# Kernel tuning notes

Measured on AMD Instinct MI355X. Metric: run time of the kernel, lower is better.

Reference implementation:

```python
import jax, jax.numpy as jnp
from jax import lax
import numpy as np


def _conv(x, w, stride):
    # x: [B,C,D,H,W], w: [3,3,3,Cin,Cout]; kernel 3, pad 1 (matches SubMConv3d / SparseConv3d(3, s, padding=1))
    return lax.conv_general_dilated(x, w, (stride, stride, stride), [(1, 1)] * 3,
                                    dimension_numbers=('NCDHW', 'DHWIO', 'NCDHW'))


def _bn_relu(y, scale, shift, mask):
    # eval-mode BatchNorm folded to scale/shift, ReLU, then restrict to active sites
    return jnp.maximum(y * scale[None, :, None, None, None] + shift[None, :, None, None, None], 0.0) * mask


def _downsample_mask(m):
    # SparseConv3d(k=3, s=2, p=1): output site active iff any input in its 3x3x3 window is active
    return lax.reduce_window(m, -jnp.inf, lax.max, (1, 1, 3, 3, 3), (1, 1, 2, 2, 2),
                             [(0, 0), (0, 0), (1, 1), (1, 1), (1, 1)])


def setup_inputs() -> dict:
    key = jax.random.key(0)
    ks = jax.random.split(key, 40)
    B, D = 1, 128
    occ = jax.random.uniform(ks[0], (B, 1, D, D, D)) < 0.05
    x = jax.random.normal(ks[1], (B, 16, D, D, D), jnp.float32) * occ

    def w(k, ci, co):
        return jax.random.normal(k, (3, 3, 3, ci, co), jnp.float32) * (1.0 / np.sqrt(27.0 * ci))

    def sc(k, c):
        return jax.random.uniform(k, (c,), jnp.float32, 0.5, 1.5)

    def sh(k, c):
        return jax.random.normal(k, (c,), jnp.float32) * 0.1

    chans = [(16, 16), (16, 16), (16, 32), (32, 32), (32, 32), (32, 64), (64, 64), (64, 64), (64, 64)]
    names = ['w0a', 'w0b', 'wd0', 'w1a', 'w1b', 'wd1', 'w2a', 'w2b', 'w2c']
    d = {'x': x, 'mask': occ}
    i = 2
    for n, (ci, co) in zip(names, chans):
        d[n] = w(ks[i], ci, co)
        d['s' + n[1:]] = sc(ks[i + 1], co)
        d['b' + n[1:]] = sh(ks[i + 2], co)
        i += 3
    return d


def reference(x, mask, w0a, s0a, b0a, w0b, s0b, b0b, wd0, sd0, bd0,
              w1a, s1a, b1a, w1b, s1b, b1b, wd1, sd1, bd1,
              w2a, s2a, b2a, w2b, s2b, b2b, w2c, s2c, b2c):
    m0 = mask.astype(x.dtype)                       # active sites at full res [B,1,128,128,128]
    h = _bn_relu(_conv(x, w0a, 1), s0a, b0a, m0)    # conv0 (subm0)
    h = _bn_relu(_conv(h, w0b, 1), s0b, b0b, m0)
    m1 = _downsample_mask(m0)                       # down0 activity [B,1,64,64,64]
    h = _bn_relu(_conv(h, wd0, 2), sd0, bd0, m1)
    h = _bn_relu(_conv(h, w1a, 1), s1a, b1a, m1)    # conv1 (subm1)
    h = _bn_relu(_conv(h, w1b, 1), s1b, b1b, m1)
    m2 = _downsample_mask(m1)                       # down1 activity [B,1,32,32,32]
    h = _bn_relu(_conv(h, wd1, 2), sd1, bd1, m2)
    h = _bn_relu(_conv(h, w2a, 1), s2a, b2a, m2)    # conv2 (subm2)
    h = _bn_relu(_conv(h, w2b, 1), s2b, b2b, m2)
    h = _bn_relu(_conv(h, w2c, 1), s2c, b2c, m2)
    return h                                        # .dense() -> [B,64,32,32,32]
```

## Files before the change

### kernel.cpp

```cpp
#include <hip/hip_runtime.h>
#include <cstdint>

typedef unsigned short u16;
typedef unsigned int u32;
typedef unsigned char u8;
typedef unsigned long long u64;
typedef __attribute__((ext_vector_type(8))) short short8;
typedef __attribute__((ext_vector_type(4))) float f32x4;

#define CAP 131072

__device__ __forceinline__ float bf1(u16 v){ union{u32 i; float f;} c; c.i = ((u32)v) << 16; return c.f; }
__device__ __forceinline__ u16 f2bf(float f){
    union{float f; u32 i;} c; c.f = f; u32 i = c.i;
    return (u16)((i + 0x7FFFu + ((i >> 16) & 1u)) >> 16);
}
__device__ __forceinline__ u16 bits2bf(u32 b){ union{u32 i; float f;} c; c.i = b; return f2bf(c.f); }

constexpr int ilog2c(int n){ return n <= 1 ? 0 : 1 + ilog2c(n / 2); }

struct PAll {
    const void* w[9];
    u32 wstart[10];
    int cin[9], cout[9], mode[9];
    const void* s[18];
};

__global__ __launch_bounds__(256)
void prepact_k(PAll J, u16* __restrict__ FR, float* __restrict__ S,
               const u16* __restrict__ s0a_probe, u32* __restrict__ flag,
               const void* __restrict__ xv, u64* __restrict__ bmask,
               u32* __restrict__ bcnt, u16* __restrict__ Xp){
    int ok = 1;
    #pragma unroll
    for (int i = 0; i < 8; i += 2){
        u16 vv = s0a_probe[i];
        if (vv < 0x3F00u || vv > 0x3FC0u) ok = 0;
    }
    const u32 isbf = ok ? 1u : 0u;

    if (blockIdx.x < 8192){
        const int v = blockIdx.x * 256 + threadIdx.x;
        const size_t N = 2097152;
        u16 vals[16];
        u32 a = 0;
        if (isbf) {
            const u16* x = (const u16*)xv;
            #pragma unroll
            for (int c = 0; c < 16; ++c){
                const u16 b = x[(size_t)c * N + v];
                vals[c] = b;
                a |= (u32)b & 0x7FFFu;
            }
        } else {
            const u32* x = (const u32*)xv;
            #pragma unroll
            for (int c = 0; c < 16; ++c){
                const u32 b = x[(size_t)c * N + v];
                vals[c] = bits2bf(b);
                a |= b & 0x7FFFFFFFu;
            }
        }
        const bool act = (a != 0);
        const u64 m = __ballot(act);
        __shared__ u32 wc[4];
        const int lane = threadIdx.x & 63, wv = threadIdx.x >> 6;
        if (lane == 0) { bmask[v >> 6] = m; wc[wv] = (u32)__popcll(m); }
        __syncthreads();
        if (threadIdx.x == 0) bcnt[blockIdx.x] = wc[0] + wc[1] + wc[2] + wc[3];
        if (act){
            u32 wbase = 0;
            for (int i = 0; i < wv; ++i) wbase += wc[i];
            const u32 local = wbase + (u32)__popcll(m & ((1ull << lane) - 1ull));
            u16* dst = Xp + ((size_t)blockIdx.x * 256 + local) * 16;
            *(short8*)(dst)     = *(const short8*)(vals);
            *(short8*)(dst + 8) = *(const short8*)(vals + 8);
        }
        return;
    }

    const int gi = (int)(blockIdx.x - 8192) * 256 + threadIdx.x;
    if (gi == 0) flag[0] = isbf;

    const int wtot = (int)J.wstart[9];
    if (gi < wtot){
        int j = 0;
        while (gi >= (int)J.wstart[j + 1]) ++j;
        const int i = gi - (int)J.wstart[j];
        const void* w = J.w[j];
        const int CIN = J.cin[j], COUT = J.cout[j];
        const int jj = i & 7;
        const int lane = (i >> 3) & 63;
        int rest = i >> 9;
        int src = -1;
        if (J.mode[j] == 0){
            const int KC = CIN >> 5, NT = COUT >> 4;
            const int nt = rest % NT; rest /= NT;
            const int kc = rest % KC; const int tap = rest / KC;
            const int k = kc * 32 + (lane >> 4) * 8 + jj;
            const int co = nt * 16 + (lane & 15);
            src = (tap * CIN + k) * COUT + co;
        } else if (J.mode[j] == 1){
            const int nt = rest & 1; const int pair = rest >> 1;
            const int kg = (lane >> 4) * 8 + jj;
            const int tap = pair * 2 + (kg >> 4);
            const int ci = kg & 15;
            const int co = nt * 16 + (lane & 15);
            if (tap < 27) src = (tap * 16 + ci) * 32 + co;
        } else {
            const int pair = rest;
            const int kg = (lane >> 4) * 8 + jj;
            const int tap = pair * 2 + (kg >> 4);
            const int ci = kg & 15;
            const int co = lane & 15;
            if (tap < 27) src = (tap * 16 + ci) * 16 + co;
        }
        float v = 0.f;
        if (src >= 0) v = isbf ? bf1(((const u16*)w)[src]) : ((const float*)w)[src];
        FR[gi] = f2bf(v);
    } else {
        const int i2 = gi - wtot;
        const int len[18] = {16,16,16,16,32,32,32,32,32,32,64,64,64,64,64,64,64,64};
        const int off[18] = {0,16,32,48,64,96,128,160,192,224,256,320,384,448,512,576,640,704};
        if (i2 < 768){
            int b = 0, base = 0;
            while (i2 >= base + len[b]) { base += len[b]; ++b; }
            const int t = i2 - base;
            const float v = isbf ? bf1(((const u16*)J.s[b])[t]) : ((const float*)J.s[b])[t];
            S[off[b] + t] = v;
        }
    }
}

__global__ __launch_bounds__(1024)
void aux_k(const u32* __restrict__ bcnt, u32* __restrict__ boff, u32* __restrict__ cnt,
           const u64* __restrict__ bmask, u8* __restrict__ m1){
    if (blockIdx.x == 0){
        __shared__ u32 lds[1024];
        const int t = threadIdx.x;
        u32 loc[8]; u32 s = 0;
        #pragma unroll
        for (int i = 0; i < 8; ++i){ loc[i] = s; s += bcnt[t * 8 + i]; }
        lds[t] = s;
        __syncthreads();
        u32 v = s;
        for (int d = 1; d < 1024; d <<= 1){
            u32 o = (t >= d) ? lds[t - d] : 0;
            __syncthreads();
            v += o; lds[t] = v;
            __syncthreads();
        }
        const u32 base = v - s;
        #pragma unroll
        for (int i = 0; i < 8; ++i) boff[t * 8 + i] = base + loc[i];
        if (t == 1023) cnt[0] = v;
    } else {
        const int v = (blockIdx.x - 1) * 1024 + threadIdx.x;
        const int xo = v & 63, yo = (v >> 6) & 63, zo = v >> 12;
        u32 a = 0;
        #pragma unroll
        for (int kz = 0; kz < 3; ++kz){ const int iz = 2*zo + kz - 1; if ((unsigned)iz >= 128u) continue;
          #pragma unroll
          for (int ky = 0; ky < 3; ++ky){ const int iy = 2*yo + ky - 1; if ((unsigned)iy >= 128u) continue;
            #pragma unroll
            for (int kx = 0; kx < 3; ++kx){ const int ix = 2*xo + kx - 1; if ((unsigned)ix >= 128u) continue;
              const int vv = (iz * 128 + iy) * 128 + ix;
              a |= (u32)((bmask[vv >> 6] >> (vv & 63)) & 1ull);
        }}}
        m1[v] = (u8)a;
    }
}

__global__ __launch_bounds__(256)
void scatter2m_k(const u16* __restrict__ Xp, const u64* __restrict__ bmask,
                 const u32* __restrict__ boff, int* __restrict__ idxmap,
                 int* __restrict__ alist, u16* __restrict__ f,
                 const u8* __restrict__ m1, u8* __restrict__ m2){
    if (blockIdx.x < 8192){
        const int v = blockIdx.x * 256 + threadIdx.x;
        const int lane = threadIdx.x & 63, wv = threadIdx.x >> 6;
        const u64 m = bmask[v >> 6];
        __shared__ u32 wc[4];
        if (lane == 0) wc[wv] = (u32)__popcll(m);
        __syncthreads();
        u32 wbase = 0;
        for (int i = 0; i < wv; ++i) wbase += wc[i];
        const bool act = (m >> lane) & 1ull;
        const u32 rank = (u32)__popcll(m & ((1ull << lane) - 1ull));
        int slot = -1;
        if (act){
            const u32 sl = boff[blockIdx.x] + wbase + rank;
            if (sl < CAP){
                slot = (int)sl;
                alist[slot] = v;
                const u16* src = Xp + ((size_t)blockIdx.x * 256 + wbase + rank) * 16;
                u16* dst = f + (size_t)slot * 16;
                *(short8*)(dst)     = *(const short8*)(src);
                *(short8*)(dst + 8) = *(const short8*)(src + 8);
            }
        }
        idxmap[v] = slot;
    } else {
        const int v = (int)(blockIdx.x - 8192) * 256 + threadIdx.x;
        const int xo = v & 31, yo = (v >> 5) & 31, zo = v >> 10;
        u8 a = 0;
        #pragma unroll
        for (int kz = 0; kz < 3; ++kz){ const int iz = 2*zo + kz - 1; if ((unsigned)iz >= 64u) continue;
          #pragma unroll
          for (int ky = 0; ky < 3; ++ky){ const int iy = 2*yo + ky - 1; if ((unsigned)iy >= 64u) continue;
            #pragma unroll
            for (int kx = 0; kx < 3; ++kx){ const int ix = 2*xo + kx - 1; if ((unsigned)ix >= 64u) continue;
              a |= m1[((size_t)iz * 64 + iy) * 64 + ix];
        }}}
        m2[v] = a;
    }
}

__global__ __launch_bounds__(256)
void sconvm_k(const u16* __restrict__ fin, const int* __restrict__ idxmap,
              const int* __restrict__ alist, const u32* __restrict__ cnt,
              const u16* __restrict__ wf, const float* __restrict__ sc,
              const float* __restrict__ sh, u16* __restrict__ fout){
    const int n = min((int)cnt[0], CAP);
    const int j = blockIdx.x * 4 + (threadIdx.x >> 6);
    const int sbase = j * 16;
    if (sbase >= n) return;
    const int lane = threadIdx.x & 63;
    const int m = lane & 15, quad = lane >> 4;

    const int s = sbase + m;
    const int v = (s < n) ? alist[s] : -1;
    int xo = 0, yo = 0, zo = 0;
    if (v >= 0){ xo = v & 127; yo = (v >> 7) & 127; zo = v >> 14; }

    f32x4 acc = {0.f,0.f,0.f,0.f};
    #pragma unroll
    for (int p = 0; p < 14; ++p){
        const int tp = p * 2 + (quad >> 1);
        short8 a = {0,0,0,0,0,0,0,0};
        if (v >= 0 && tp < 27){
            const int kz = tp / 9, ky = (tp / 3) % 3, kx = tp % 3;
            const int iz = zo + kz - 1, iy = yo + ky - 1, ix = xo + kx - 1;
            if ((unsigned)iz < 128u && (unsigned)iy < 128u && (unsigned)ix < 128u){
                const int sn = idxmap[((size_t)iz * 128 + iy) * 128 + ix];
                if (sn >= 0) a = *(const short8*)(fin + (size_t)sn * 16 + (quad & 1) * 8);
            }
        }
        short8 b = *(const short8*)(wf + ((size_t)p * 64 + lane) * 8);
        acc = __builtin_amdgcn_mfma_f32_16x16x32_bf16(a, b, acc, 0, 0, 0);
    }

    const int co = lane & 15;
    const float scl = sc[co], shf = sh[co];
    #pragma unroll
    for (int r = 0; r < 4; ++r){
        const int srow = sbase + quad * 4 + r;
        if (srow < n){
            fout[(size_t)srow * 16 + co] = f2bf(fmaxf(acc[r] * scl + shf, 0.f));
        }
    }
}

__global__ __launch_bounds__(256)
void convd0m_k(const u16* __restrict__ fbuf, const int* __restrict__ idxmap,
               const u16* __restrict__ wf, const float* __restrict__ sc,
               const float* __restrict__ sh, const u8* __restrict__ mk,
               u16* __restrict__ out)
{
    const int wj = blockIdx.x * 4 + (threadIdx.x >> 6);
    const int lane = threadIdx.x & 63;
    const int m = lane & 15, quad = lane >> 4;
    const int xo_b = (wj & 3) * 16;
    const int yo = (wj >> 2) & 63;
    const int zo = wj >> 8;

    f32x4 acc0 = {0.f,0.f,0.f,0.f}, acc1 = {0.f,0.f,0.f,0.f};
    const int ix_m = (xo_b + m) * 2 - 1;

    #pragma unroll
    for (int p = 0; p < 14; ++p){
        const int tp = p * 2 + (quad >> 1);
        short8 a = {0,0,0,0,0,0,0,0};
        if (tp < 27){
            const int kz = tp / 9, ky = (tp / 3) % 3, kx = tp % 3;
            const int iz = 2*zo + kz - 1, iy = 2*yo + ky - 1, ix = ix_m + kx;
            if ((unsigned)iz < 128u && (unsigned)iy < 128u && (unsigned)ix < 128u){
                const int sn = idxmap[((size_t)iz * 128 + iy) * 128 + ix];
                if (sn >= 0) a = *(const short8*)(fbuf + (size_t)sn * 16 + (quad & 1) * 8);
            }
        }
        short8 b0 = *(const short8*)(wf + ((size_t)(p*2+0) * 64 + lane) * 8);
        short8 b1 = *(const short8*)(wf + ((size_t)(p*2+1) * 64 + lane) * 8);
        acc0 = __builtin_amdgcn_mfma_f32_16x16x32_bf16(a, b0, acc0, 0, 0, 0);
        acc1 = __builtin_amdgcn_mfma_f32_16x16x32_bf16(a, b1, acc1, 0, 0, 0);
    }

    const int vb = wj * 16 + quad * 4;
    const u32 m4 = *(const u32*)(mk + vb);
    const int n = lane & 15;
    #pragma unroll
    for (int nt = 0; nt < 2; ++nt){
        const int co = nt * 16 + n;
        const float s = sc[co], h = sh[co];
        const f32x4 acc = nt ? acc1 : acc0;
        #pragma unroll
        for (int r = 0; r < 4; ++r){
            float val = fmaxf(acc[r] * s + h, 0.f);
            val = ((m4 >> (8*r)) & 0xFFu) ? val : 0.f;
            out[(size_t)(vb + r) * 32 + co] = f2bf(val);
        }
    }
}

template<int DIN, int DOUT, int CIN, int COUT, int STRIDE, bool FINAL>
__global__ __launch_bounds__(256)
void mconv_k(const u16* __restrict__ in, const u16* __restrict__ wf,
             const float* __restrict__ sc, const float* __restrict__ sh,
             const u8* __restrict__ mk, void* __restrict__ out,
             const u32* __restrict__ flag)
{
    constexpr int KC = CIN / 32;
    constexpr int NT = COUT / 16;
    constexpr int XT = DOUT / 16;
    const int wj = blockIdx.x * 4 + (threadIdx.x >> 6);
    const int lane = threadIdx.x & 63;
    const int m = lane & 15, quad = lane >> 4;

    const int xo_b = (wj % XT) * 16;
    const int yo = (wj / XT) % DOUT;
    const int zo = wj / (XT * DOUT);

    f32x4 acc[NT];
    #pragma unroll
    for (int i = 0; i < NT; ++i) acc[i] = (f32x4){0.f,0.f,0.f,0.f};

    const int ix0 = (xo_b + m) * STRIDE - 1;
    for (int kz = 0; kz < 3; ++kz){
      const int iz = zo * STRIDE + kz - 1;
      if ((unsigned)iz >= (unsigned)DIN) continue;
      for (int ky = 0; ky < 3; ++ky){
        const int iy = yo * STRIDE + ky - 1;
        if ((unsigned)iy >= (unsigned)DIN) continue;
        const size_t rowb = ((size_t)iz * DIN + iy) * DIN;
        #pragma unroll
        for (int kx = 0; kx < 3; ++kx){
          const int ix = ix0 + kx;
          const bool v = (unsigned)ix < (unsigned)DIN;
          const int tap = (kz*3 + ky)*3 + kx;
          const u16* ap = in + (rowb + ix) * CIN + quad * 8;
          const u16* bp = wf + (size_t)tap * KC * NT * 512 + lane * 8;
          #pragma unroll
          for (int kc = 0; kc < KC; ++kc){
            short8 a = {0,0,0,0,0,0,0,0};
            if (v) a = *(const short8*)(ap + kc * 32);
            #pragma unroll
            for (int nt = 0; nt < NT; ++nt){
              short8 b = *(const short8*)(bp + (kc * NT + nt) * 512);
              acc[nt] = __builtin_amdgcn_mfma_f32_16x16x32_bf16(a, b, acc[nt], 0, 0, 0);
            }
          }
    }}}

    const int vb = wj * 16 + quad * 4;
    const u32 m4 = *(const u32*)(mk + vb);
    const int n = lane & 15;
    #pragma unroll
    for (int nt = 0; nt < NT; ++nt){
        const int co = nt * 16 + n;
        const float s = sc[co], h = sh[co];
        #pragma unroll
        for (int r = 0; r < 4; ++r){
            float val = fmaxf(acc[nt][r] * s + h, 0.f);
            val = ((m4 >> (8*r)) & 0xFFu) ? val : 0.f;
            ((u16*)out)[(size_t)(vb + r) * COUT + co] = f2bf(val);
        }
    }
    (void)flag;
}

template<int D, int CIN, int COUT, bool FINAL>
__global__ __launch_bounds__((D/32)*4*64)
void mconvw_k(const u16* __restrict__ in, const u16* __restrict__ wf,
              const float* __restrict__ sc, const float* __restrict__ sh,
              const u8* __restrict__ mk, void* __restrict__ out,
              const u32* __restrict__ flag)
{
    constexpr int KC = CIN / 32;
    constexpr int NT = COUT / 16;
    constexpr int CH8 = CIN / 8;
    constexpr int WPR = D / 32;
    constexpr int BT = WPR * 4 * 64;
    __shared__ u16 tile[16 * 2048];

    const int t = threadIdx.x;
    const int yp = blockIdx.x % (D / 2);
    const int zp = blockIdx.x / (D / 2);

    #pragma unroll
    for (int ri = 0; ri < 16; ++ri){
        const int dz = ri >> 2, jy = ri & 3;
        const int iz = 2*zp + dz - 1, iy = 2*yp + jy - 1;
        if ((unsigned)iz < (unsigned)D && (unsigned)iy < (unsigned)D){
            const u16* src = in + ((size_t)(iz * D + iy) * D) * CIN;
            u16* dst = &tile[ri * 2048];
            for (int c = t; c < D * CH8; c += BT){
                const int x = c / CH8, c8 = c % CH8;
                *(short8*)(dst + (c8 * D + x) * 8) = *(const short8*)(src + c * 8);
            }
        }
    }
    __syncthreads();

    const int lane = t & 63, w = t >> 6;
    const int r = w / WPR;
    const int r2z = r >> 1, r2y = r & 1;
    const int xo_b = (w % WPR) * 32;
    const int zo = 2*zp + r2z, yo = 2*yp + r2y;
    const int m = lane & 15, quad = lane >> 4;

    f32x4 acc0[NT], acc1[NT];
    #pragma unroll
    for (int i = 0; i < NT; ++i){ acc0[i] = (f32x4){0.f,0.f,0.f,0.f}; acc1[i] = (f32x4){0.f,0.f,0.f,0.f}; }

    #pragma unroll
    for (int kz = 0; kz < 3; ++kz){
      const int iz = zo + kz - 1;
      if ((unsigned)iz >= (unsigned)D) continue;
      #pragma unroll
      for (int ky = 0; ky < 3; ++ky){
        const int iy = yo + ky - 1;
        if ((unsigned)iy >= (unsigned)D) continue;
        const u16* row = &tile[((r2z + kz) * 4 + (r2y + ky)) * 2048];
        #pragma unroll
        for (int kx = 0; kx < 3; ++kx){
          const int ix0 = xo_b + m + kx - 1;
          const int ix1 = ix0 + 16;
          const bool aok0 = (unsigned)ix0 < (unsigned)D;
          const bool aok1 = (unsigned)ix1 < (unsigned)D;
          const int tap = (kz * 3 + ky) * 3 + kx;
          const u16* bp = wf + (size_t)tap * KC * NT * 512 + lane * 8;
          #pragma unroll
          for (int kc = 0; kc < KC; ++kc){
            short8 a0 = {0,0,0,0,0,0,0,0};
            short8 a1 = {0,0,0,0,0,0,0,0};
            if (aok0) a0 = *(const short8*)(row + ((kc * 4 + quad) * D + ix0) * 8);
            if (aok1) a1 = *(const short8*)(row + ((kc * 4 + quad) * D + ix1) * 8);
            #pragma unroll
            for (int nt = 0; nt < NT; ++nt){
              short8 b = *(const short8*)(bp + (kc * NT + nt) * 512);
              acc0[nt] = __builtin_amdgcn_mfma_f32_16x16x32_bf16(a0, b, acc0[nt], 0, 0, 0);
              acc1[nt] = __builtin_amdgcn_mfma_f32_16x16x32_bf16(a1, b, acc1[nt], 0, 0, 0);
            }
          }
        }
      }
    }

    const int base = (zo * D + yo) * D;
    const int vb0 = base + xo_b + quad * 4;
    const int vb1 = vb0 + 16;
    const u32 m4_0 = *(const u32*)(mk + vb0);
    const u32 m4_1 = *(const u32*)(mk + vb1);
    const int n = lane & 15;
    if (FINAL) {
        const bool bfout = flag[0] != 0;
        #pragma unroll
        for (int nt = 0; nt < NT; ++nt){
            const int co = nt * 16 + n;
            const float s = sc[co], h = sh[co];
            float4 o0, o1;
            float* p0 = &o0.x; float* p1 = &o1.x;
            #pragma unroll
            for (int r4 = 0; r4 < 4; ++r4){
                float v0 = fmaxf(acc0[nt][r4] * s + h, 0.f);
                float v1 = fmaxf(acc1[nt][r4] * s + h, 0.f);
                p0[r4] = ((m4_0 >> (8*r4)) & 0xFFu) ? v0 : 0.f;
                p1[r4] = ((m4_1 >> (8*r4)) & 0xFFu) ? v1 : 0.f;
            }
            if (!bfout) {
                *(float4*)((float*)out + (size_t)co * (D*D*D) + vb0) = o0;
                *(float4*)((float*)out + (size_t)co * (D*D*D) + vb1) = o1;
            } else {
                u16* ob0 = (u16*)out + (size_t)co * (D*D*D) + vb0;
                u16* ob1 = (u16*)out + (size_t)co * (D*D*D) + vb1;
                #pragma unroll
                for (int r4 = 0; r4 < 4; ++r4){ ob0[r4] = f2bf(p0[r4]); ob1[r4] = f2bf(p1[r4]); }
            }
        }
    } else {
        #pragma unroll
        for (int nt = 0; nt < NT; ++nt){
            const int co = nt * 16 + n;
            const float s = sc[co], h = sh[co];
            #pragma unroll
            for (int r4 = 0; r4 < 4; ++r4){
                float v0 = fmaxf(acc0[nt][r4] * s + h, 0.f);
                float v1 = fmaxf(acc1[nt][r4] * s + h, 0.f);
                v0 = ((m4_0 >> (8*r4)) & 0xFFu) ? v0 : 0.f;
                v1 = ((m4_1 >> (8*r4)) & 0xFFu) ? v1 : 0.f;
                ((u16*)out)[(size_t)(vb0 + r4) * COUT + co] = f2bf(v0);
                ((u16*)out)[(size_t)(vb1 + r4) * COUT + co] = f2bf(v1);
            }
        }
    }
}

extern "C" void kernel_launch(void* const* d_in, const int* in_sizes, int n_in,
                              void* d_out, int out_size, void* d_ws, size_t ws_size,
                              hipStream_t stream)
{
    (void)out_size; (void)ws_size;

    int wb = 2;
    for (int i = 1; i < n_in; ++i) { if (in_sizes[i] == 6912) { wb = i; break; } }

    const void* x = d_in[0];
    const void *w0a=d_in[wb+0],  *s0a=d_in[wb+1],  *b0a=d_in[wb+2];
    const void *w0b=d_in[wb+3],  *s0b=d_in[wb+4],  *b0b=d_in[wb+5];
    const void *wd0=d_in[wb+6],  *sd0=d_in[wb+7],  *bd0=d_in[wb+8];
    const void *w1a=d_in[wb+9],  *s1a=d_in[wb+10], *b1a=d_in[wb+11];
    const void *w1b=d_in[wb+12], *s1b=d_in[wb+13], *b1b=d_in[wb+14];
    const void *wd1=d_in[wb+15], *sd1=d_in[wb+16], *bd1=d_in[wb+17];
    const void *w2a=d_in[wb+18], *s2a=d_in[wb+19], *b2a=d_in[wb+20];
    const void *w2b=d_in[wb+21], *s2b=d_in[wb+22], *b2b=d_in[wb+23];
    const void *w2c=d_in[wb+24], *s2c=d_in[wb+25], *b2c=d_in[wb+26];

    char* ws = (char*)d_ws;
    int*   idxmap = (int*)(ws);
    u16*   Fb0    = (u16*)(ws + 8388608);
    u16*   Fb1    = (u16*)(ws + 12582912);
    u16*   Fb2    = (u16*)(ws + 16777216);
    u16*   Rb1    = (u16*)(ws + 25165824);
    u16*   Rb2    = (u16*)(ws + 41943040);
    u8*    m1     = (u8*)(ws + 58720256);
    u8*    m2     = (u8*)(ws + 58982400);
    u32*   cnt    = (u32*)(ws + 59015168);
    int*   alist  = (int*)(ws + 59015424);
    u16*   FR     = (u16*)(ws + 59539712);
    float* S      = (float*)(ws + 60483328);
    u32*   flag   = (u32*)(ws + 60486400);
    u64*   bmask  = (u64*)(ws + 60486656);
    u32*   bcnt   = (u32*)(ws + 60748800);
    u32*   boff   = (u32*)(ws + 60781568);
    u16*   Xp     = (u16*)(ws + 67108864);

    u16* wfs0a = FR + 0;
    u16* wfs0b = FR + 7168;
    u16* fd0   = FR + 14336;
    u16* f1a   = FR + 28672;
    u16* f1b   = FR + 56320;
    u16* fd1   = FR + 83968;
    u16* f2a   = FR + 139264;
    u16* f2b   = FR + 249856;
    u16* f2c   = FR + 360448;

    PAll J;
    const void* jsrc[9] = {w0a, w0b, wd0, w1a, w1b, wd1, w2a, w2b, w2c};
    const u32 jlen[9]   = {7168,7168,14336,27648,27648,55296,110592,110592,110592};
    const int jcin[9]   = {16,16,16,32,32,32,64,64,64};
    const int jcout[9]  = {16,16,32,32,32,64,64,64,64};
    const int jmode[9]  = {2,2,1,0,0,0,0,0,0};
    u32 acc = 0;
    for (int i = 0; i < 9; ++i){
        J.w[i] = jsrc[i]; J.wstart[i] = acc; acc += jlen[i];
        J.cin[i] = jcin[i]; J.cout[i] = jcout[i]; J.mode[i] = jmode[i];
    }
    J.wstart[9] = acc;
    const void* sv[18] = {s0a,b0a,s0b,b0b,sd0,bd0,s1a,b1a,s1b,b1b,sd1,bd1,s2a,b2a,s2b,b2b,s2c,b2c};
    for (int i = 0; i < 18; ++i) J.s[i] = sv[i];
    const u32 ptot = acc + 768;
    const int prep_blocks = (int)((ptot + 255) / 256);

    float *cs0a=S+0,  *cb0a=S+16,  *cs0b=S+32,  *cb0b=S+48;
    float *csd0=S+64, *cbd0=S+96,  *cs1a=S+128, *cb1a=S+160, *cs1b=S+192, *cb1b=S+224;
    float *csd1=S+256,*cbd1=S+320, *cs2a=S+384, *cb2a=S+448, *cs2b=S+512, *cb2b=S+576, *cs2c=S+640, *cb2c=S+704;

    prepact_k<<<8192 + prep_blocks, 256, 0, stream>>>(J, FR, S, (const u16*)s0a, flag,
                                                      x, bmask, bcnt, Xp);
    aux_k<<<257, 1024, 0, stream>>>(bcnt, boff, cnt, bmask, m1);
    scatter2m_k<<<8320, 256, 0, stream>>>(Xp, bmask, boff, idxmap, alist, Fb0, m1, m2);

    sconvm_k<<<2048, 256, 0, stream>>>(Fb0, idxmap, alist, cnt, wfs0a, cs0a, cb0a, Fb1);
    sconvm_k<<<2048, 256, 0, stream>>>(Fb1, idxmap, alist, cnt, wfs0b, cs0b, cb0b, Fb2);
    convd0m_k<<<4096, 256, 0, stream>>>(Fb2, idxmap, fd0, csd0, cbd0, m1, Rb1);
    mconvw_k<64,32,32,false><<<1024, 512, 0, stream>>>(Rb1, f1a, cs1a, cb1a, m1, Rb2, flag);
    mconvw_k<64,32,32,false><<<1024, 512, 0, stream>>>(Rb2, f1b, cs1b, cb1b, m1, Rb1, flag);
    mconv_k<64,32,32,64,2,false><<<512, 256, 0, stream>>>(Rb1, fd1, csd1, cbd1, m2, Rb2, flag);
    mconvw_k<32,64,64,false><<<256, 256, 0, stream>>>(Rb2, f2a, cs2a, cb2a, m2, Rb1, flag);
    mconvw_k<32,64,64,false><<<256, 256, 0, stream>>>(Rb1, f2b, cs2b, cb2b, m2, Rb2, flag);
    mconvw_k<32,64,64,true ><<<256, 256, 0, stream>>>(Rb2, f2c, cs2c, cb2c, m2, d_out, flag);
}
```

Measured before the change: 485.2 us.

## Replace block scan with atomic offsets and fuse tail convs into cooperative kernel

Removes the separate aux kernel's block-count prefix scan by having each block reserve its compaction slots with an atomicAdd on a global counter. Computes m2 directly from the full-resolution bitmask instead of from m1, so m1 and m2 are built in the same scatter kernel. Fuses the last four dense 32^3 convolutions into one cooperative kernel separated by grid syncs, cutting launch overhead. The trade-offs are that the compacted slot order becomes nondeterministic, and the tail now runs on only 256 blocks, with grid-sync overhead added between stages.

```diff
diff --git a/kernel.cpp b/kernel.cpp
--- a/kernel.cpp
+++ b/kernel.cpp
@@ -1,5 +1,8 @@
 #include <hip/hip_runtime.h>
+#include <hip/hip_cooperative_groups.h>
 #include <cstdint>
+
+namespace cg = cooperative_groups;
 
 typedef unsigned short u16;
 typedef unsigned int u32;
@@ -17,8 +20,6 @@
 }
 __device__ __forceinline__ u16 bits2bf(u32 b){ union{u32 i; float f;} c; c.i = b; return f2bf(c.f); }
 
-constexpr int ilog2c(int n){ return n <= 1 ? 0 : 1 + ilog2c(n / 2); }
-
 struct PAll {
     const void* w[9];
     u32 wstart[10];
@@ -30,7 +31,7 @@
 void prepact_k(PAll J, u16* __restrict__ FR, float* __restrict__ S,
                const u16* __restrict__ s0a_probe, u32* __restrict__ flag,
                const void* __restrict__ xv, u64* __restrict__ bmask,
-               u32* __restrict__ bcnt, u16* __restrict__ Xp){
+               u32* __restrict__ cnt, u16* __restrict__ Xp){
     int ok = 1;
     #pragma unroll
     for (int i = 0; i < 8; i += 2){
@@ -67,7 +68,6 @@
         const int lane = threadIdx.x & 63, wv = threadIdx.x >> 6;
         if (lane == 0) { bmask[v >> 6] = m; wc[wv] = (u32)__popcll(m); }
         __syncthreads();
-        if (threadIdx.x == 0) bcnt[blockIdx.x] = wc[0] + wc[1] + wc[2] + wc[3];
         if (act){
             u32 wbase = 0;
             for (int i = 0; i < wv; ++i) wbase += wc[i];
@@ -80,7 +80,7 @@
     }
 
     const int gi = (int)(blockIdx.x - 8192) * 256 + threadIdx.x;
-    if (gi == 0) flag[0] = isbf;
+    if (gi == 0) { flag[0] = isbf; cnt[0] = 0; }
 
     const int wtot = (int)J.wstart[9];
     if (gi < wtot){
@@ -132,30 +132,40 @@
     }
 }
 
-__global__ __launch_bounds__(1024)
-void aux_k(const u32* __restrict__ bcnt, u32* __restrict__ boff, u32* __restrict__ cnt,
-           const u64* __restrict__ bmask, u8* __restrict__ m1){
-    if (blockIdx.x == 0){
-        __shared__ u32 lds[1024];
-        const int t = threadIdx.x;
-        u32 loc[8]; u32 s = 0;
-        #pragma unroll
-        for (int i = 0; i < 8; ++i){ loc[i] = s; s += bcnt[t * 8 + i]; }
-        lds[t] = s;
+__global__ __launch_bounds__(256)
+void scatter2m_k(const u16* __restrict__ Xp, const u64* __restrict__ bmask,
+                 int* __restrict__ idxmap, int* __restrict__ alist,
+                 u16* __restrict__ f, u32* __restrict__ cnt,
+                 u8* __restrict__ m1, u8* __restrict__ m2){
+    if (blockIdx.x < 8192){
+        const int v = blockIdx.x * 256 + threadIdx.x;
+        const int lane = threadIdx.x & 63, wv = threadIdx.x >> 6;
+        const u64 m = bmask[v >> 6];
+        __shared__ u32 wc[4];
+        __shared__ u32 sbase;
+        if (lane == 0) wc[wv] = (u32)__popcll(m);
         __syncthreads();
-        u32 v = s;
-        for (int d = 1; d < 1024; d <<= 1){
-            u32 o = (t >= d) ? lds[t - d] : 0;
-            __syncthreads();
-            v += o; lds[t] = v;
-            __syncthreads();
-        }
-        const u32 base = v - s;
-        #pragma unroll
-        for (int i = 0; i < 8; ++i) boff[t * 8 + i] = base + loc[i];
-        if (t == 1023) cnt[0] = v;
-    } else {
-        const int v = (blockIdx.x - 1) * 1024 + threadIdx.x;
+        if (threadIdx.x == 0) sbase = atomicAdd(cnt, wc[0] + wc[1] + wc[2] + wc[3]);
+        __syncthreads();
+        u32 wbase = 0;
+        for (int i = 0; i < wv; ++i) wbase += wc[i];
+        const bool act = (m >> lane) & 1ull;
+        const u32 rank = (u32)__popcll(m & ((1ull << lane) - 1ull));
+        int slot = -1;
+        if (act){
+            const u32 sl = sbase + wbase + rank;
+            if (sl < CAP){
+                slot = (int)sl;
+                alist[slot] = v;
+                const u16* src = Xp + ((size_t)blockIdx.x * 256 + wbase + rank) * 16;
+                u16* dst = f + (size_t)slot * 16;
+                *(short8*)(dst)     = *(const short8*)(src);
+                *(short8*)(dst + 8) = *(const short8*)(src + 8);
+            }
+        }
+        idxmap[v] = slot;
+    } else if (blockIdx.x < 8192 + 1024){
+        const int v = (int)(blockIdx.x - 8192) * 256 + threadIdx.x;
         const int xo = v & 63, yo = (v >> 6) & 63, zo = v >> 12;
         u32 a = 0;
         #pragma unroll
@@ -168,51 +178,30 @@
               a |= (u32)((bmask[vv >> 6] >> (vv & 63)) & 1ull);
         }}}
         m1[v] = (u8)a;
-    }
-}
-
-__global__ __launch_bounds__(256)
-void scatter2m_k(const u16* __restrict__ Xp, const u64* __restrict__ bmask,
-                 const u32* __restrict__ boff, int* __restrict__ idxmap,
-                 int* __restrict__ alist, u16* __restrict__ f,
-                 const u8* __restrict__ m1, u8* __restrict__ m2){
-    if (blockIdx.x < 8192){
-        const int v = blockIdx.x * 256 + threadIdx.x;
-        const int lane = threadIdx.x & 63, wv = threadIdx.x >> 6;
-        const u64 m = bmask[v >> 6];
-        __shared__ u32 wc[4];
-        if (lane == 0) wc[wv] = (u32)__popcll(m);
-        __syncthreads();
-        u32 wbase = 0;
-        for (int i = 0; i < wv; ++i) wbase += wc[i];
-        const bool act = (m >> lane) & 1ull;
-        const u32 rank = (u32)__popcll(m & ((1ull << lane) - 1ull));
-        int slot = -1;
-        if (act){
-            const u32 sl = boff[blockIdx.x] + wbase + rank;
-            if (sl < CAP){
-                slot = (int)sl;
-                alist[slot] = v;
-                const u16* src = Xp + ((size_t)blockIdx.x * 256 + wbase + rank) * 16;
-                u16* dst = f + (size_t)slot * 16;
-                *(short8*)(dst)     = *(const short8*)(src);
-                *(short8*)(dst + 8) = *(const short8*)(src + 8);
-            }
-        }
-        idxmap[v] = slot;
     } else {
-        const int v = (int)(blockIdx.x - 8192) * 256 + threadIdx.x;
+        const int v = (int)(blockIdx.x - 9216) * 256 + threadIdx.x;
         const int xo = v & 31, yo = (v >> 5) & 31, zo = v >> 10;
-        u8 a = 0;
-        #pragma unroll
-        for (int kz = 0; kz < 3; ++kz){ const int iz = 2*zo + kz - 1; if ((unsigned)iz >= 64u) continue;
+        const int xlo = max(0, 4*xo - 3), xhi = min(127, 4*xo + 3);
+        const int w0 = xlo >> 6, w1 = xhi >> 6;
+        u32 a = 0;
+        #pragma unroll
+        for (int dz = -3; dz <= 3; ++dz){ const int iz = 4*zo + dz; if ((unsigned)iz >= 128u) continue;
           #pragma unroll
-          for (int ky = 0; ky < 3; ++ky){ const int iy = 2*yo + ky - 1; if ((unsigned)iy >= 64u) continue;
-            #pragma unroll
-            for (int kx = 0; kx < 3; ++kx){ const int ix = 2*xo + kx - 1; if ((unsigned)ix >= 64u) continue;
-              a |= m1[((size_t)iz * 64 + iy) * 64 + ix];
-        }}}
-        m2[v] = a;
+          for (int dy = -3; dy <= 3; ++dy){ const int iy = 4*yo + dy; if ((unsigned)iy >= 128u) continue;
+            const int rw = (iz * 128 + iy) >> 6 << 1;
+            const int rowword = ((iz * 128 + iy) * 128) >> 6;
+            if (w0 == w1){
+                const u64 mw = bmask[rowword + w0];
+                const int sh = xlo & 63, len = xhi - xlo + 1;
+                if ((mw >> sh) & ((1ull << len) - 1ull)) a = 1;
+            } else {
+                const u64 lo = bmask[rowword + w0] >> (xlo & 63);
+                const u64 hi = bmask[rowword + w1] & ((1ull << ((xhi & 63) + 1)) - 1ull);
+                if (lo | hi) a = 1;
+            }
+            (void)rw;
+        }}
+        m2[v] = (u8)a;
     }
 }
 
@@ -310,72 +299,6 @@
             out[(size_t)(vb + r) * 32 + co] = f2bf(val);
         }
     }
-}
-
-template<int DIN, int DOUT, int CIN, int COUT, int STRIDE, bool FINAL>
-__global__ __launch_bounds__(256)
-void mconv_k(const u16* __restrict__ in, const u16* __restrict__ wf,
-             const float* __restrict__ sc, const float* __restrict__ sh,
-             const u8* __restrict__ mk, void* __restrict__ out,
-             const u32* __restrict__ flag)
-{
-    constexpr int KC = CIN / 32;
-    constexpr int NT = COUT / 16;
-    constexpr int XT = DOUT / 16;
-    const int wj = blockIdx.x * 4 + (threadIdx.x >> 6);
-    const int lane = threadIdx.x & 63;
-    const int m = lane & 15, quad = lane >> 4;
-
-    const int xo_b = (wj % XT) * 16;
-    const int yo = (wj / XT) % DOUT;
-    const int zo = wj / (XT * DOUT);
-
-    f32x4 acc[NT];
-    #pragma unroll
-    for (int i = 0; i < NT; ++i) acc[i] = (f32x4){0.f,0.f,0.f,0.f};
-
-    const int ix0 = (xo_b + m) * STRIDE - 1;
-    for (int kz = 0; kz < 3; ++kz){
-      const int iz = zo * STRIDE + kz - 1;
-      if ((unsigned)iz >= (unsigned)DIN) continue;
-      for (int ky = 0; ky < 3; ++ky){
-        const int iy = yo * STRIDE + ky - 1;
-        if ((unsigned)iy >= (unsigned)DIN) continue;
-        const size_t rowb = ((size_t)iz * DIN + iy) * DIN;
-        #pragma unroll
-        for (int kx = 0; kx < 3; ++kx){
-          const int ix = ix0 + kx;
-          const bool v = (unsigned)ix < (unsigned)DIN;
-          const int tap = (kz*3 + ky)*3 + kx;
-          const u16* ap = in + (rowb + ix) * CIN + quad * 8;
-          const u16* bp = wf + (size_t)tap * KC * NT * 512 + lane * 8;
-          #pragma unroll
-          for (int kc = 0; kc < KC; ++kc){
-            short8 a = {0,0,0,0,0,0,0,0};
-            if (v) a = *(const short8*)(ap + kc * 32);
-            #pragma unroll
-            for (int nt = 0; nt < NT; ++nt){
-              short8 b = *(const short8*)(bp + (kc * NT + nt) * 512);
-              acc[nt] = __builtin_amdgcn_mfma_f32_16x16x32_bf16(a, b, acc[nt], 0, 0, 0);
-            }
-          }
-    }}}
-
-    const int vb = wj * 16 + quad * 4;
-    const u32 m4 = *(const u32*)(mk + vb);
-    const int n = lane & 15;
-    #pragma unroll
-    for (int nt = 0; nt < NT; ++nt){
-        const int co = nt * 16 + n;
-        const float s = sc[co], h = sh[co];
-        #pragma unroll
-        for (int r = 0; r < 4; ++r){
-            float val = fmaxf(acc[nt][r] * s + h, 0.f);
-            val = ((m4 >> (8*r)) & 0xFFu) ? val : 0.f;
-            ((u16*)out)[(size_t)(vb + r) * COUT + co] = f2bf(val);
-        }
-    }
-    (void)flag;
 }
 
 template<int D, int CIN, int COUT, bool FINAL>
@@ -462,6 +385,81 @@
     const u32 m4_0 = *(const u32*)(mk + vb0);
     const u32 m4_1 = *(const u32*)(mk + vb1);
     const int n = lane & 15;
+    #pragma unroll
+    for (int nt = 0; nt < NT; ++nt){
+        const int co = nt * 16 + n;
+        const float s = sc[co], h = sh[co];
+        #pragma unroll
+        for (int r4 = 0; r4 < 4; ++r4){
+            float v0 = fmaxf(acc0[nt][r4] * s + h, 0.f);
+            float v1 = fmaxf(acc1[nt][r4] * s + h, 0.f);
+            v0 = ((m4_0 >> (8*r4)) & 0xFFu) ? v0 : 0.f;
+            v1 = ((m4_1 >> (8*r4)) & 0xFFu) ? v1 : 0.f;
+            ((u16*)out)[(size_t)(vb0 + r4) * COUT + co] = f2bf(v0);
+            ((u16*)out)[(size_t)(vb1 + r4) * COUT + co] = f2bf(v1);
+        }
+    }
+    (void)flag;
+}
+
+template<int DIN, int CIN, int COUT, int STRIDE, bool FINAL>
+__device__ __forceinline__ void tconv(const u16* __restrict__ in, const u16* __restrict__ wf,
+                                      const float* __restrict__ sc, const float* __restrict__ sh,
+                                      const u8* __restrict__ mk, void* __restrict__ out,
+                                      const u32* __restrict__ flag)
+{
+    constexpr int KC = CIN / 32;
+    constexpr int NT = COUT / 16;
+    const int wid = blockIdx.x * 4 + (threadIdx.x >> 6);
+    const int lane = threadIdx.x & 63;
+    const int m = lane & 15, quad = lane >> 4;
+    const int yo = wid & 31, zo = wid >> 5;
+
+    f32x4 acc0[NT], acc1[NT];
+    #pragma unroll
+    for (int i = 0; i < NT; ++i){ acc0[i] = (f32x4){0.f,0.f,0.f,0.f}; acc1[i] = (f32x4){0.f,0.f,0.f,0.f}; }
+
+    const int ixA0 = m * STRIDE - 1;
+    const int ixB0 = (m + 16) * STRIDE - 1;
+
+    #pragma unroll
+    for (int kz = 0; kz < 3; ++kz){
+      const int iz = zo * STRIDE + kz - 1;
+      if ((unsigned)iz >= (unsigned)DIN) continue;
+      #pragma unroll
+      for (int ky = 0; ky < 3; ++ky){
+        const int iy = yo * STRIDE + ky - 1;
+        if ((unsigned)iy >= (unsigned)DIN) continue;
+        const size_t rowb = ((size_t)iz * DIN + iy) * DIN;
+        #pragma unroll
+        for (int kx = 0; kx < 3; ++kx){
+          const int ixA = ixA0 + kx, ixB = ixB0 + kx;
+          const bool vA = (unsigned)ixA < (unsigned)DIN;
+          const bool vB = (unsigned)ixB < (unsigned)DIN;
+          const int tap = (kz * 3 + ky) * 3 + kx;
+          const u16* bp = wf + (size_t)tap * KC * NT * 512 + lane * 8;
+          #pragma unroll
+          for (int kc = 0; kc < KC; ++kc){
+            short8 a0 = {0,0,0,0,0,0,0,0};
+            short8 a1 = {0,0,0,0,0,0,0,0};
+            if (vA) a0 = *(const short8*)(in + (rowb + ixA) * CIN + kc * 32 + quad * 8);
+            if (vB) a1 = *(const short8*)(in + (rowb + ixB) * CIN + kc * 32 + quad * 8);
+            #pragma unroll
+            for (int nt = 0; nt < NT; ++nt){
+              short8 b = *(const short8*)(bp + (kc * NT + nt) * 512);
+              acc0[nt] = __builtin_amdgcn_mfma_f32_16x16x32_bf16(a0, b, acc0[nt], 0, 0, 0);
+              acc1[nt] = __builtin_amdgcn_mfma_f32_16x16x32_bf16(a1, b, acc1[nt], 0, 0, 0);
+            }
+          }
+        }
+      }
+    }
+
+    const int vb0 = wid * 32 + quad * 4;
+    const int vb1 = vb0 + 16;
+    const u32 m4_0 = *(const u32*)(mk + vb0);
+    const u32 m4_1 = *(const u32*)(mk + vb1);
+    const int n = lane & 15;
     if (FINAL) {
         const bool bfout = flag[0] != 0;
         #pragma unroll
@@ -478,11 +476,11 @@
                 p1[r4] = ((m4_1 >> (8*r4)) & 0xFFu) ? v1 : 0.f;
             }
             if (!bfout) {
-                *(float4*)((float*)out + (size_t)co * (D*D*D) + vb0) = o0;
-                *(float4*)((float*)out + (size_t)co * (D*D*D) + vb1) = o1;
+                *(float4*)((float*)out + (size_t)co * 32768 + vb0) = o0;
+                *(float4*)((float*)out + (size_t)co * 32768 + vb1) = o1;
             } else {
-                u16* ob0 = (u16*)out + (size_t)co * (D*D*D) + vb0;
-                u16* ob1 = (u16*)out + (size_t)co * (D*D*D) + vb1;
+                u16* ob0 = (u16*)out + (size_t)co * 32768 + vb0;
+                u16* ob1 = (u16*)out + (size_t)co * 32768 + vb1;
                 #pragma unroll
                 for (int r4 = 0; r4 < 4; ++r4){ ob0[r4] = f2bf(p0[r4]); ob1[r4] = f2bf(p1[r4]); }
             }
@@ -503,6 +501,26 @@
             }
         }
     }
+}
+
+__global__ __launch_bounds__(256)
+void tail_k(const u16* __restrict__ dn_in, u16* __restrict__ t0, u16* __restrict__ t1,
+            u16* __restrict__ t2, const u16* __restrict__ wd1f, const u16* __restrict__ w2af,
+            const u16* __restrict__ w2bf, const u16* __restrict__ w2cf,
+            const float* __restrict__ S, const u8* __restrict__ m2,
+            void* __restrict__ outp, const u32* __restrict__ flag)
+{
+    cg::grid_group g = cg::this_grid();
+    tconv<64, 32, 64, 2, false>(dn_in, wd1f, S + 256, S + 320, m2, t0, flag);
+    __threadfence();
+    g.sync();
+    tconv<32, 64, 64, 1, false>(t0, w2af, S + 384, S + 448, m2, t1, flag);
+    __threadfence();
+    g.sync();
+    tconv<32, 64, 64, 1, false>(t1, w2bf, S + 512, S + 576, m2, t2, flag);
+    __threadfence();
+    g.sync();
+    tconv<32, 64, 64, 1, true >(t2, w2cf, S + 640, S + 704, m2, outp, flag);
 }
 
 extern "C" void kernel_launch(void* const* d_in, const int* in_sizes, int n_in,
@@ -540,8 +558,6 @@
     float* S      = (float*)(ws + 60483328);
     u32*   flag   = (u32*)(ws + 60486400);
     u64*   bmask  = (u64*)(ws + 60486656);
-    u32*   bcnt   = (u32*)(ws + 60748800);
-    u32*   boff   = (u32*)(ws + 60781568);
     u16*   Xp     = (u16*)(ws + 67108864);
 
     u16* wfs0a = FR + 0;
@@ -573,20 +589,21 @@
 
     float *cs0a=S+0,  *cb0a=S+16,  *cs0b=S+32,  *cb0b=S+48;
     float *csd0=S+64, *cbd0=S+96,  *cs1a=S+128, *cb1a=S+160, *cs1b=S+192, *cb1b=S+224;
-    float *csd1=S+256,*cbd1=S+320, *cs2a=S+384, *cb2a=S+448, *cs2b=S+512, *cb2b=S+576, *cs2c=S+640, *cb2c=S+704;
 
     prepact_k<<<8192 + prep_blocks, 256, 0, stream>>>(J, FR, S, (const u16*)s0a, flag,
-                                                      x, bmask, bcnt, Xp);
-    aux_k<<<257, 1024, 0, stream>>>(bcnt, boff, cnt, bmask, m1);
-    scatter2m_k<<<8320, 256, 0, stream>>>(Xp, bmask, boff, idxmap, alist, Fb0, m1, m2);
+                                                      x, bmask, cnt, Xp);
+    scatter2m_k<<<9344, 256, 0, stream>>>(Xp, bmask, idxmap, alist, Fb0, cnt, m1, m2);
 
     sconvm_k<<<2048, 256, 0, stream>>>(Fb0, idxmap, alist, cnt, wfs0a, cs0a, cb0a, Fb1);
     sconvm_k<<<2048, 256, 0, stream>>>(Fb1, idxmap, alist, cnt, wfs0b, cs0b, cb0b, Fb2);
     convd0m_k<<<4096, 256, 0, stream>>>(Fb2, idxmap, fd0, csd0, cbd0, m1, Rb1);
     mconvw_k<64,32,32,false><<<1024, 512, 0, stream>>>(Rb1, f1a, cs1a, cb1a, m1, Rb2, flag);
     mconvw_k<64,32,32,false><<<1024, 512, 0, stream>>>(Rb2, f1b, cs1b, cb1b, m1, Rb1, flag);
-    mconv_k<64,32,32,64,2,false><<<512, 256, 0, stream>>>(Rb1, fd1, csd1, cbd1, m2, Rb2, flag);
-    mconvw_k<32,64,64,false><<<256, 256, 0, stream>>>(Rb2, f2a, cs2a, cb2a, m2, Rb1, flag);
-    mconvw_k<32,64,64,false><<<256, 256, 0, stream>>>(Rb1, f2b, cs2b, cb2b, m2, Rb2, flag);
-    mconvw_k<32,64,64,true ><<<256, 256, 0, stream>>>(Rb2, f2c, cs2c, cb2c, m2, d_out, flag);
-}
+
+    const u16* a_dn = Rb1; u16* a_t0 = Rb2; u16* a_t1 = Fb0; u16* a_t2 = Fb1;
+    const u16* a_w0 = fd1; const u16* a_w1 = f2a; const u16* a_w2 = f2b; const u16* a_w3 = f2c;
+    const float* a_S = S; const u8* a_m2 = m2; void* a_out = d_out; const u32* a_flag = flag;
+    void* targs[12] = { &a_dn, &a_t0, &a_t1, &a_t2, &a_w0, &a_w1, &a_w2, &a_w3,
+                        &a_S, &a_m2, &a_out, &a_flag };
+    hipLaunchCooperativeKernel((void*)tail_k, dim3(256), dim3(256), targs, 0, stream);
+}
```

Measured after the change: 804.4 us. 65.8% more time.

## Replace prefix-scan kernel with atomic slot allocation and compute m2 from bitmask

Applied to the files above, without the earlier changes.

Drops the separate aux_k launch that did a block-count prefix scan and the m1 downsample. Each scatter block now reserves its output range with one atomicAdd on a counter that prepact_k zeroes. The m1 computation moves into scatter2m_k as extra blocks, and m2 is computed straight from the full-resolution bitmask over a 7x7x7 window instead of reading m1, which removes the m1-to-m2 dependency. This saves a kernel launch and a serial scan, but active-site order now depends on atomic timing, so output slot assignment is nondeterministic.

```diff
diff --git a/kernel.cpp b/kernel.cpp
--- a/kernel.cpp
+++ b/kernel.cpp
@@ -17,8 +17,6 @@
 }
 __device__ __forceinline__ u16 bits2bf(u32 b){ union{u32 i; float f;} c; c.i = b; return f2bf(c.f); }
 
-constexpr int ilog2c(int n){ return n <= 1 ? 0 : 1 + ilog2c(n / 2); }
-
 struct PAll {
     const void* w[9];
     u32 wstart[10];
@@ -30,7 +28,7 @@
 void prepact_k(PAll J, u16* __restrict__ FR, float* __restrict__ S,
                const u16* __restrict__ s0a_probe, u32* __restrict__ flag,
                const void* __restrict__ xv, u64* __restrict__ bmask,
-               u32* __restrict__ bcnt, u16* __restrict__ Xp){
+               u32* __restrict__ cnt, u16* __restrict__ Xp){
     int ok = 1;
     #pragma unroll
     for (int i = 0; i < 8; i += 2){
@@ -67,7 +65,6 @@
         const int lane = threadIdx.x & 63, wv = threadIdx.x >> 6;
         if (lane == 0) { bmask[v >> 6] = m; wc[wv] = (u32)__popcll(m); }
         __syncthreads();
-        if (threadIdx.x == 0) bcnt[blockIdx.x] = wc[0] + wc[1] + wc[2] + wc[3];
         if (act){
             u32 wbase = 0;
             for (int i = 0; i < wv; ++i) wbase += wc[i];
@@ -80,7 +77,7 @@
     }
 
     const int gi = (int)(blockIdx.x - 8192) * 256 + threadIdx.x;
-    if (gi == 0) flag[0] = isbf;
+    if (gi == 0) { flag[0] = isbf; cnt[0] = 0; }
 
     const int wtot = (int)J.wstart[9];
     if (gi < wtot){
@@ -132,56 +129,20 @@
     }
 }
 
-__global__ __launch_bounds__(1024)
-void aux_k(const u32* __restrict__ bcnt, u32* __restrict__ boff, u32* __restrict__ cnt,
-           const u64* __restrict__ bmask, u8* __restrict__ m1){
-    if (blockIdx.x == 0){
-        __shared__ u32 lds[1024];
-        const int t = threadIdx.x;
-        u32 loc[8]; u32 s = 0;
-        #pragma unroll
-        for (int i = 0; i < 8; ++i){ loc[i] = s; s += bcnt[t * 8 + i]; }
-        lds[t] = s;
-        __syncthreads();
-        u32 v = s;
-        for (int d = 1; d < 1024; d <<= 1){
-            u32 o = (t >= d) ? lds[t - d] : 0;
-            __syncthreads();
-            v += o; lds[t] = v;
-            __syncthreads();
-        }
-        const u32 base = v - s;
-        #pragma unroll
-        for (int i = 0; i < 8; ++i) boff[t * 8 + i] = base + loc[i];
-        if (t == 1023) cnt[0] = v;
-    } else {
-        const int v = (blockIdx.x - 1) * 1024 + threadIdx.x;
-        const int xo = v & 63, yo = (v >> 6) & 63, zo = v >> 12;
-        u32 a = 0;
-        #pragma unroll
-        for (int kz = 0; kz < 3; ++kz){ const int iz = 2*zo + kz - 1; if ((unsigned)iz >= 128u) continue;
-          #pragma unroll
-          for (int ky = 0; ky < 3; ++ky){ const int iy = 2*yo + ky - 1; if ((unsigned)iy >= 128u) continue;
-            #pragma unroll
-            for (int kx = 0; kx < 3; ++kx){ const int ix = 2*xo + kx - 1; if ((unsigned)ix >= 128u) continue;
-              const int vv = (iz * 128 + iy) * 128 + ix;
-              a |= (u32)((bmask[vv >> 6] >> (vv & 63)) & 1ull);
-        }}}
-        m1[v] = (u8)a;
-    }
-}
-
 __global__ __launch_bounds__(256)
 void scatter2m_k(const u16* __restrict__ Xp, const u64* __restrict__ bmask,
-                 const u32* __restrict__ boff, int* __restrict__ idxmap,
-                 int* __restrict__ alist, u16* __restrict__ f,
-                 const u8* __restrict__ m1, u8* __restrict__ m2){
+                 int* __restrict__ idxmap, int* __restrict__ alist,
+                 u16* __restrict__ f, u32* __restrict__ cnt,
+                 u8* __restrict__ m1, u8* __restrict__ m2){
     if (blockIdx.x < 8192){
         const int v = blockIdx.x * 256 + threadIdx.x;
         const int lane = threadIdx.x & 63, wv = threadIdx.x >> 6;
         const u64 m = bmask[v >> 6];
         __shared__ u32 wc[4];
+        __shared__ u32 sbase;
         if (lane == 0) wc[wv] = (u32)__popcll(m);
+        __syncthreads();
+        if (threadIdx.x == 0) sbase = atomicAdd(cnt, wc[0] + wc[1] + wc[2] + wc[3]);
         __syncthreads();
         u32 wbase = 0;
         for (int i = 0; i < wv; ++i) wbase += wc[i];
@@ -189,7 +150,7 @@
         const u32 rank = (u32)__popcll(m & ((1ull << lane) - 1ull));
         int slot = -1;
         if (act){
-            const u32 sl = boff[blockIdx.x] + wbase + rank;
+            const u32 sl = sbase + wbase + rank;
             if (sl < CAP){
                 slot = (int)sl;
                 alist[slot] = v;
@@ -200,19 +161,42 @@
             }
         }
         idxmap[v] = slot;
+    } else if (blockIdx.x < 8192 + 1024){
+        const int v = (int)(blockIdx.x - 8192) * 256 + threadIdx.x;
+        const int xo = v & 63, yo = (v >> 6) & 63, zo = v >> 12;
+        u32 a = 0;
+        #pragma unroll
+        for (int kz = 0; kz < 3; ++kz){ const int iz = 2*zo + kz - 1; if ((unsigned)iz >= 128u) continue;
+          #pragma unroll
+          for (int ky = 0; ky < 3; ++ky){ const int iy = 2*yo + ky - 1; if ((unsigned)iy >= 128u) continue;
+            #pragma unroll
+            for (int kx = 0; kx < 3; ++kx){ const int ix = 2*xo + kx - 1; if ((unsigned)ix >= 128u) continue;
+              const int vv = (iz * 128 + iy) * 128 + ix;
+              a |= (u32)((bmask[vv >> 6] >> (vv & 63)) & 1ull);
+        }}}
+        m1[v] = (u8)a;
     } else {
-        const int v = (int)(blockIdx.x - 8192) * 256 + threadIdx.x;
+        const int v = (int)(blockIdx.x - 9216) * 256 + threadIdx.x;
         const int xo = v & 31, yo = (v >> 5) & 31, zo = v >> 10;
-        u8 a = 0;
-        #pragma unroll
-        for (int kz = 0; kz < 3; ++kz){ const int iz = 2*zo + kz - 1; if ((unsigned)iz >= 64u) continue;
+        const int xlo = max(0, 4*xo - 3), xhi = min(127, 4*xo + 3);
+        const int w0 = xlo >> 6, w1 = xhi >> 6;
+        u32 a = 0;
+        #pragma unroll
+        for (int dz = -3; dz <= 3; ++dz){ const int iz = 4*zo + dz; if ((unsigned)iz >= 128u) continue;
           #pragma unroll
-          for (int ky = 0; ky < 3; ++ky){ const int iy = 2*yo + ky - 1; if ((unsigned)iy >= 64u) continue;
-            #pragma unroll
-            for (int kx = 0; kx < 3; ++kx){ const int ix = 2*xo + kx - 1; if ((unsigned)ix >= 64u) continue;
-              a |= m1[((size_t)iz * 64 + iy) * 64 + ix];
-        }}}
-        m2[v] = a;
+          for (int dy = -3; dy <= 3; ++dy){ const int iy = 4*yo + dy; if ((unsigned)iy >= 128u) continue;
+            const int rowword = ((iz * 128 + iy) * 128) >> 6;
+            if (w0 == w1){
+                const u64 mw = bmask[rowword + w0];
+                const int sh = xlo & 63, len = xhi - xlo + 1;
+                if ((mw >> sh) & ((1ull << len) - 1ull)) a = 1;
+            } else {
+                const u64 lo = bmask[rowword + w0] >> (xlo & 63);
+                const u64 hi = bmask[rowword + w1] & ((1ull << ((xhi & 63) + 1)) - 1ull);
+                if (lo | hi) a = 1;
+            }
+        }}
+        m2[v] = (u8)a;
     }
 }
 
@@ -540,8 +524,6 @@
     float* S      = (float*)(ws + 60483328);
     u32*   flag   = (u32*)(ws + 60486400);
     u64*   bmask  = (u64*)(ws + 60486656);
-    u32*   bcnt   = (u32*)(ws + 60748800);
-    u32*   boff   = (u32*)(ws + 60781568);
     u16*   Xp     = (u16*)(ws + 67108864);
 
     u16* wfs0a = FR + 0;
@@ -576,9 +558,8 @@
     float *csd1=S+256,*cbd1=S+320, *cs2a=S+384, *cb2a=S+448, *cs2b=S+512, *cb2b=S+576, *cs2c=S+640, *cb2c=S+704;
 
     prepact_k<<<8192 + prep_blocks, 256, 0, stream>>>(J, FR, S, (const u16*)s0a, flag,
-                                                      x, bmask, bcnt, Xp);
-    aux_k<<<257, 1024, 0, stream>>>(bcnt, boff, cnt, bmask, m1);
-    scatter2m_k<<<8320, 256, 0, stream>>>(Xp, bmask, boff, idxmap, alist, Fb0, m1, m2);
+                                                      x, bmask, cnt, Xp);
+    scatter2m_k<<<9344, 256, 0, stream>>>(Xp, bmask, idxmap, alist, Fb0, cnt, m1, m2);
 
     sconvm_k<<<2048, 256, 0, stream>>>(Fb0, idxmap, alist, cnt, wfs0a, cs0a, cb0a, Fb1);
     sconvm_k<<<2048, 256, 0, stream>>>(Fb1, idxmap, alist, cnt, wfs0b, cs0b, cb0b, Fb2);
```

After: 572.8 us. 18.1% more time.
